# Kernel optimization log

Measured on AMD Instinct MI355X. Metric: run time of the kernel, lower is better.

The kernel has to match this reference:

```python
import jax, jax.numpy as jnp
import numpy as np

B, C, H, W = 32, 3, 512, 512
MIN_STR, MEAN_STR = 1.0, 5.0


def setup_inputs() -> dict:
    key = jax.random.key(0)
    k1, k2, k3, k4, k5 = jax.random.split(key, 5)
    x = jax.random.uniform(k1, (B, C, H, W), dtype=jnp.float32)  # images in [0,1]
    phases = 2.0 * jnp.pi * jax.random.uniform(k2, (B * C,), dtype=jnp.float32)
    strengths = jax.random.exponential(k3, (B, C), dtype=jnp.float32) * MEAN_STR + MIN_STR
    idx_h = jax.random.randint(k4, (B * C,), 0, H)
    idx_w = jax.random.randint(k5, (B * C,), 0, W)
    return {"x": x, "phases": phases, "strengths": strengths,
            "idx_h": idx_h, "idx_w": idx_w}


def reference(x, phases, strengths, idx_h, idx_w):
    b, c, h, w = x.shape
    # torch pairing: arange(b).repeat(c) -> i % b ; arange(c).repeat(b) -> i % c
    i = jnp.arange(b * c)
    bi = i % b
    ci = i % c
    # sparse scatter of one frequency bin per (b,c) plane
    mag = jnp.zeros_like(x).at[bi, ci, idx_h, idx_w].set(1.0)
    ph = jnp.zeros_like(x).at[bi, ci, idx_h, idx_w].set(phases)
    noise = jax.lax.complex(mag, ph)
    # symmetrize by index-reversal flip over spatial dims (as in torch .flip)
    noise = noise + jnp.flip(noise, axis=(2, 3))
    # N-D inverse FFT over spatial dims, keep real part
    w_ft = jnp.fft.ifftn(noise, axes=(2, 3)).real.astype(x.dtype)
    # L2-normalize each (b,c) plane
    norm = jnp.sqrt(jnp.sum(w_ft * w_ft, axis=(2, 3), keepdims=True))
    w_ft = w_ft / norm
    scale = max(h, w) / 32.0  # static python scalar
    out = x + scale * strengths[:, :, None, None] * w_ft
    return jnp.clip(out, 0.0, 1.0)
```

## Files before the change

### kernel.cpp

```cpp
#include <hip/hip_runtime.h>
#include <math.h>


namespace {

constexpr int H = 512, W = 512, B = 32, C = 3;
constexpr int ROWS = 8;
constexpr int TPB = 256;

typedef float floatx4 __attribute__((ext_vector_type(4)));

__global__ __launch_bounds__(TPB) void fourier_noise_kernel(
    const float* __restrict__ xin,
    const float* __restrict__ phases,
    const float* __restrict__ strengths,
    const int* __restrict__ idx_h,
    const int* __restrict__ idx_w,
    float* __restrict__ out)
{
    const int pl = blockIdx.y;
    const int b  = pl / C;
    const int c  = pl % C;

    int d = (c - b) % 3; if (d < 0) d += 3;
    const int k = (2 * d) % 3;
    const int i = b + B * k;

    const int   h0 = idx_h[i];
    const int   w0 = idx_w[i];
    const float p  = phases[i];
    const float st = strengths[b * C + c];

    const float halfE = 0.5f * (1.0f + p * p);
    const float s1 = (((h0 & 255) == 0) && ((w0 & 255) == 0)) ? 1.0f : halfE;
    const float s2 = ((h0 == 255 || h0 == 511) && (w0 == 255 || w0 == 511)) ? 1.0f : halfE;
    const float S  = s1 + s2;
    const float g = (16.0f / 512.0f) * st * rsqrtf(S);

    const int h0r = 511 - h0;
    const int w0r = 511 - w0;
    constexpr float STEP = 6.28318530717958647692f / 512.0f;

    __shared__ floatx4 rowtab[ROWS];
    const int row0 = blockIdx.x * ROWS;
    if (threadIdx.x < ROWS) {
        const int y = row0 + threadIdx.x;
        float sy1, cy1, sy2, cy2;
        sincosf(float((h0  * y) & 511) * STEP, &sy1, &cy1);
        sincosf(float((h0r * y) & 511) * STEP, &sy2, &cy2);
        floatx4 rt;
        rt.x = fmaf(-p, sy1, cy1);
        rt.y = -fmaf(p, cy1, sy1);
        rt.z = fmaf(-p, sy2, cy2);
        rt.w = -fmaf(p, cy2, sy2);
        rowtab[threadIdx.x] = rt;
    }

    const int xg   = (threadIdx.x & 127) << 2;
    const int rsub = threadIdx.x >> 7;
    const size_t plane_off = (size_t)pl * (size_t)(H * W);

    const size_t off0 = plane_off + (size_t)(row0 + 0 + rsub) * W + (size_t)xg;
    const size_t off1 = plane_off + (size_t)(row0 + 2 + rsub) * W + (size_t)xg;
    const size_t off2 = plane_off + (size_t)(row0 + 4 + rsub) * W + (size_t)xg;
    const size_t off3 = plane_off + (size_t)(row0 + 6 + rsub) * W + (size_t)xg;
    const floatx4 vi0 = *reinterpret_cast<const floatx4*>(xin + off0);
    const floatx4 vi1 = *reinterpret_cast<const floatx4*>(xin + off1);
    const floatx4 vi2 = *reinterpret_cast<const floatx4*>(xin + off2);
    const floatx4 vi3 = *reinterpret_cast<const floatx4*>(xin + off3);

    float cx1[4], sx1[4], cx2[4], sx2[4];
#pragma unroll
    for (int j = 0; j < 4; ++j) {
        const int xx = xg + j;
        sincosf(float((w0  * xx) & 511) * STEP, &sx1[j], &cx1[j]);
        sincosf(float((w0r * xx) & 511) * STEP, &sx2[j], &cx2[j]);
    }

    __syncthreads();

#define DO_ROW(vi, off, it)                                                     \
    {                                                                           \
        const floatx4 ab = rowtab[(it) * 2 + rsub]; \
        floatx4 vo;                                                             \
        _Pragma("unroll")                                                       \
        for (int j = 0; j < 4; ++j) {                                           \
            float v = cx1[j] * ab.x + sx1[j] * ab.y                             \
                    + cx2[j] * ab.z + sx2[j] * ab.w;                            \
            vo[j] = fminf(fmaxf(fmaf(g, v, vi[j]), 0.0f), 1.0f);                \
        }                                                                       \
        __builtin_nontemporal_store(vo, reinterpret_cast<floatx4*>(out + off)); \
    }

    DO_ROW(vi0, off0, 0)
    DO_ROW(vi1, off1, 1)
    DO_ROW(vi2, off2, 2)
    DO_ROW(vi3, off3, 3)
#undef DO_ROW
}

}

extern "C" void kernel_launch(void* const* d_in, const int* in_sizes, int n_in,
                              void* d_out, int out_size, void* d_ws, size_t ws_size,
                              hipStream_t stream) {
    const float* x         = (const float*)d_in[0];
    const float* phases    = (const float*)d_in[1];
    const float* strengths = (const float*)d_in[2];
    const int*   idx_h     = (const int*)d_in[3];
    const int*   idx_w     = (const int*)d_in[4];
    float*       out       = (float*)d_out;

    dim3 grid(H / ROWS, B * C);
    fourier_noise_kernel<<<grid, dim3(TPB), 0, stream>>>(
        x, phases, strengths, idx_h, idx_w, out);
}
```

Baseline: 182.0 us.

## Compute row twiddles per thread with hardware sin/cos, drop shared table and barrier

Removes the shared-memory row table and its __syncthreads. Each thread now computes its own four row twiddles using the AMDGCN hardware sin/cos intrinsics, which take the angle in revolutions, in place of library sincosf. Offsets switch to 32-bit arithmetic, and the input loads are issued before the parameter loads and trig so their latency overlaps compute. In exchange there is redundant per-thread trig work, and the hardware sin/cos may be less accurate than sincosf.

```diff
diff --git a/kernel.cpp b/kernel.cpp
--- a/kernel.cpp
+++ b/kernel.cpp
@@ -18,75 +18,73 @@
     const int* __restrict__ idx_w,
     float* __restrict__ out)
 {
-    const int pl = blockIdx.y;
-    const int b  = pl / C;
-    const int c  = pl % C;
-
-    int d = (c - b) % 3; if (d < 0) d += 3;
-    const int k = (2 * d) % 3;
-    const int i = b + B * k;
-
-    const int   h0 = idx_h[i];
-    const int   w0 = idx_w[i];
-    const float p  = phases[i];
-    const float st = strengths[b * C + c];
-
-    const float halfE = 0.5f * (1.0f + p * p);
-    const float s1 = (((h0 & 255) == 0) && ((w0 & 255) == 0)) ? 1.0f : halfE;
-    const float s2 = ((h0 == 255 || h0 == 511) && (w0 == 255 || w0 == 511)) ? 1.0f : halfE;
-    const float S  = s1 + s2;
-    const float g = (16.0f / 512.0f) * st * rsqrtf(S);
-
-    const int h0r = 511 - h0;
-    const int w0r = 511 - w0;
-    constexpr float STEP = 6.28318530717958647692f / 512.0f;
-
-    __shared__ floatx4 rowtab[ROWS];
+    const int pl   = blockIdx.y;
     const int row0 = blockIdx.x * ROWS;
-    if (threadIdx.x < ROWS) {
-        const int y = row0 + threadIdx.x;
-        float sy1, cy1, sy2, cy2;
-        sincosf(float((h0  * y) & 511) * STEP, &sy1, &cy1);
-        sincosf(float((h0r * y) & 511) * STEP, &sy2, &cy2);
-        floatx4 rt;
-        rt.x = fmaf(-p, sy1, cy1);
-        rt.y = -fmaf(p, cy1, sy1);
-        rt.z = fmaf(-p, sy2, cy2);
-        rt.w = -fmaf(p, cy2, sy2);
-        rowtab[threadIdx.x] = rt;
-    }
-
     const int xg   = (threadIdx.x & 127) << 2;
     const int rsub = threadIdx.x >> 7;
-    const size_t plane_off = (size_t)pl * (size_t)(H * W);
 
-    const size_t off0 = plane_off + (size_t)(row0 + 0 + rsub) * W + (size_t)xg;
-    const size_t off1 = plane_off + (size_t)(row0 + 2 + rsub) * W + (size_t)xg;
-    const size_t off2 = plane_off + (size_t)(row0 + 4 + rsub) * W + (size_t)xg;
-    const size_t off3 = plane_off + (size_t)(row0 + 6 + rsub) * W + (size_t)xg;
+    const uint32_t off0 = (uint32_t)pl * (uint32_t)(H * W)
+                        + (uint32_t)(row0 + rsub) * (uint32_t)W + (uint32_t)xg;
+    const uint32_t off1 = off0 + 2u * W;
+    const uint32_t off2 = off0 + 4u * W;
+    const uint32_t off3 = off0 + 6u * W;
     const floatx4 vi0 = *reinterpret_cast<const floatx4*>(xin + off0);
     const floatx4 vi1 = *reinterpret_cast<const floatx4*>(xin + off1);
     const floatx4 vi2 = *reinterpret_cast<const floatx4*>(xin + off2);
     const floatx4 vi3 = *reinterpret_cast<const floatx4*>(xin + off3);
 
+    const int b = pl / C;
+    const int c = pl % C;
+    int d = (c - b) % 3; if (d < 0) d += 3;
+    const int i = b + B * ((2 * d) % 3);
+
+    const int   h0 = idx_h[i];
+    const int   w0 = idx_w[i];
+    const float p  = phases[i];
+    const float st = strengths[pl];
+
+    const float halfE = 0.5f * (1.0f + p * p);
+    const float s1 = (((h0 & 255) == 0) && ((w0 & 255) == 0)) ? 1.0f : halfE;
+    const float s2 = ((h0 == 255 || h0 == 511) && (w0 == 255 || w0 == 511)) ? 1.0f : halfE;
+    const float g  = (16.0f / 512.0f) * st * rsqrtf(s1 + s2);
+
+    const int h0r = 511 - h0;
+    const int w0r = 511 - w0;
+    constexpr float INV = 1.0f / 512.0f;
+
     float cx1[4], sx1[4], cx2[4], sx2[4];
 #pragma unroll
     for (int j = 0; j < 4; ++j) {
         const int xx = xg + j;
-        sincosf(float((w0  * xx) & 511) * STEP, &sx1[j], &cx1[j]);
-        sincosf(float((w0r * xx) & 511) * STEP, &sx2[j], &cx2[j]);
+        const float a1 = (float)((w0  * xx) & 511) * INV;
+        const float a2 = (float)((w0r * xx) & 511) * INV;
+        sx1[j] = __builtin_amdgcn_sinf(a1);
+        cx1[j] = __builtin_amdgcn_cosf(a1);
+        sx2[j] = __builtin_amdgcn_sinf(a2);
+        cx2[j] = __builtin_amdgcn_cosf(a2);
     }
 
-    __syncthreads();
+    float A1[4], B1[4], A2[4], B2[4];
+#pragma unroll
+    for (int it = 0; it < 4; ++it) {
+        const int y = row0 + rsub + 2 * it;
+        const float a1 = (float)((h0  * y) & 511) * INV;
+        const float a2 = (float)((h0r * y) & 511) * INV;
+        const float sy1 = __builtin_amdgcn_sinf(a1);
+        const float cy1 = __builtin_amdgcn_cosf(a1);
+        const float sy2 = __builtin_amdgcn_sinf(a2);
+        const float cy2 = __builtin_amdgcn_cosf(a2);
+        A1[it] = fmaf(-p, sy1, cy1);  B1[it] = -fmaf(p, cy1, sy1);
+        A2[it] = fmaf(-p, sy2, cy2);  B2[it] = -fmaf(p, cy2, sy2);
+    }
 
 #define DO_ROW(vi, off, it)                                                     \
     {                                                                           \
-        const floatx4 ab = rowtab[(it) * 2 + rsub]; \
         floatx4 vo;                                                             \
         _Pragma("unroll")                                                       \
         for (int j = 0; j < 4; ++j) {                                           \
-            float v = cx1[j] * ab.x + sx1[j] * ab.y                             \
-                    + cx2[j] * ab.z + sx2[j] * ab.w;                            \
+            float v = cx1[j] * A1[it] + sx1[j] * B1[it]                         \
+                    + cx2[j] * A2[it] + sx2[j] * B2[it];                        \
             vo[j] = fminf(fmaxf(fmaf(g, v, vi[j]), 0.0f), 1.0f);                \
         }                                                                       \
         __builtin_nontemporal_store(vo, reinterpret_cast<floatx4*>(out + off)); \
```

New measurement: 181.7 us. Within noise of the previous version (-0.1%).
